# Optimization experiments

Hardware: AMD Instinct MI355X
Metric: run time of the kernel (lower is better)

The kernel has to match this reference:

```python
import jax, jax.numpy as jnp
import numpy as np

B, T, D = 32, 2048, 80
K1 = K2 = 3
S1 = S2 = 2
CB_DIM, CB_SIZE = 512, 1024
MASK_P = 0.1
NOISE_STD = 0.1
INPUT_DIM = D * K1 * K2  # 720


def _win_idx(T_in, k, s):
    Tp = (T_in - k) // s + 1
    return jnp.arange(Tp)[:, None] * s + jnp.arange(k)[None, :]  # (Tp, k)


def _unfold(x, k, s):
    # matches torch x.unfold(1, k, s).view(B, Tp, -1): out[b, t, f*k + j] = x[b, t*s + j, f]
    idx = _win_idx(x.shape[1], k, s)
    w = x[:, idx, :]                 # (B, Tp, k, F)
    w = jnp.swapaxes(w, 2, 3)        # (B, Tp, F, k)
    return w.reshape(w.shape[0], w.shape[1], -1)


def setup_inputs() -> dict:
    key = jax.random.key(0)
    k1, k2, k3, k4, k5 = jax.random.split(key, 5)
    raw_feats = jax.random.normal(k1, (B, T, D), jnp.float32)
    auged_feats = jax.random.normal(k2, (B, T, D), jnp.float32)
    length = jax.random.randint(k3, (B,), T // 2, T + 1)
    xav = (2.0 / (INPUT_DIM + CB_DIM)) ** 0.5  # xavier_normal std
    projector = jax.random.normal(k4, (INPUT_DIM, CB_DIM), jnp.float32) * xav
    codebook = jax.random.normal(k5, (CB_SIZE, CB_DIM), jnp.float32)
    return {"raw_feats": raw_feats, "auged_feats": auged_feats, "length": length,
            "projector": projector, "codebook": codebook}


def reference(raw_feats, auged_feats, length, projector, codebook):
    T1 = (T - K1) // S1 + 1
    T2 = (T1 - K2) // S2 + 1
    idx1 = _win_idx(T, K1, S1)                         # (T1, K1)
    idx2 = _win_idx(T1, K2, S2)                        # (T2, K2)
    frame_windows = idx1[idx2].reshape(T2, K1 * K2)    # (T2, 9) original frame idx per subsampled step
    label_lengths = ((length - K1) // S1 + 1 - K2) // S2 + 1  # (B,)

    # --- label path: two torch-style unfolds -> project -> nearest codebook entry ---
    stacked = _unfold(_unfold(raw_feats, K1, S1), K2, S2)     # (B, T2, 720)
    targets = jnp.matmul(stacked, projector)                  # (B, T2, 512)
    # squared-euclidean expansion; same argmin as ||t - c||
    dist = (jnp.sum(targets * targets, axis=-1, keepdims=True)
            - 2.0 * jnp.einsum('btd,cd->btc', targets, codebook)
            + jnp.sum(codebook * codebook, axis=-1))          # (B, T2, 1024)
    labels = jnp.argmin(dist, axis=-1) + 1                    # labels start from 1; 0 = ignore idx
    valid = jnp.arange(T2)[None, :] < label_lengths[:, None]  # (B, T2)
    labels = jnp.where(valid, labels, 0)[None]                # (num_codebooks=1, B, T2)

    # --- static (span length 1) random masking on valid subsampled steps ---
    mkey = jax.random.key(42)
    km, kn = jax.random.split(mkey)
    masked = (jax.random.uniform(km, (B, T2)) < MASK_P) & valid
    masked_dim = masked.astype(jnp.float32)                   # (B, T2)
    # scatter masked subsampled steps back onto original frame indices (union of windows)
    hits = jnp.zeros((B, T), jnp.float32).at[:, frame_windows].add(masked_dim[:, :, None])
    frame_mask = hits > 0                                     # (B, T)
    noise = NOISE_STD * jax.random.normal(kn, (B, T, D), auged_feats.dtype)
    masked_feats = jnp.where(frame_mask[:, :, None], noise, auged_feats)
    return masked_feats, labels, masked_dim
```

## Files before the change

### kernel.cpp

```cpp
#include <hip/hip_runtime.h>
#include <cstdint>

#define B_    32
#define T_    2048
#define D_    80
#define T2_   511
#define NROW  16352
#define GK    720
#define CBD   512
#define CBS   1024
#define HMASK 8176
#define HN    2621440
#define NP    16384
#define KB    23

using bfrag = __attribute__((ext_vector_type(8))) short;
using f32x4 = __attribute__((ext_vector_type(4))) float;
using s4    = __attribute__((ext_vector_type(4))) short;
using s8    = __attribute__((ext_vector_type(8))) short;

__device__ inline ushort f2bf(float f){
  uint32_t u = __float_as_uint(f);
  uint32_t r = (u + 0x7FFFu + ((u >> 16) & 1u)) >> 16;
  return (ushort)r;
}
__device__ inline float bf2f(ushort h){ return __uint_as_float(((uint32_t)h) << 16); }

#define GLL16(gsrc, ldst) __builtin_amdgcn_global_load_lds( \
    (__attribute__((address_space(1))) void*)(gsrc), \
    (__attribute__((address_space(3))) void*)(ldst), 16, 0, 0)

__host__ __device__ inline uint32_t rotl_(uint32_t v, int d){ return (v<<d)|(v>>(32-d)); }

__host__ __device__ inline void tf2x32(uint32_t k0, uint32_t k1, uint32_t& x0, uint32_t& x1){
  uint32_t ks2 = k0 ^ k1 ^ 0x1BD11BDAu;
  x0 += k0; x1 += k1;
  const int r0[4] = {13,15,26,6}, r1[4] = {17,29,16,24};
#pragma unroll
  for (int i=0;i<4;i++){ x0 += x1; x1 = rotl_(x1, r0[i]); x1 ^= x0; }
  x0 += k1; x1 += ks2 + 1u;
#pragma unroll
  for (int i=0;i<4;i++){ x0 += x1; x1 = rotl_(x1, r1[i]); x1 ^= x0; }
  x0 += ks2; x1 += k0 + 2u;
#pragma unroll
  for (int i=0;i<4;i++){ x0 += x1; x1 = rotl_(x1, r0[i]); x1 ^= x0; }
  x0 += k0; x1 += k1 + 3u;
#pragma unroll
  for (int i=0;i<4;i++){ x0 += x1; x1 = rotl_(x1, r1[i]); x1 ^= x0; }
  x0 += k1; x1 += ks2 + 4u;
#pragma unroll
  for (int i=0;i<4;i++){ x0 += x1; x1 = rotl_(x1, r0[i]); x1 ^= x0; }
  x0 += ks2; x1 += k0 + 5u;
}

__device__ inline float erfinv_f(float x){
  float w = -log1pf(-x*x);
  float p;
  if (w < 5.0f){
    w -= 2.5f;
    p = 2.81022636e-08f;
    p = fmaf(p, w, 3.43273939e-07f);
    p = fmaf(p, w, -3.5233877e-06f);
    p = fmaf(p, w, -4.39150654e-06f);
    p = fmaf(p, w, 0.00021858087f);
    p = fmaf(p, w, -0.00125372503f);
    p = fmaf(p, w, -0.00417768164f);
    p = fmaf(p, w, 0.246640727f);
    p = fmaf(p, w, 1.50140941f);
  } else {
    w = sqrtf(w) - 3.0f;
    p = -0.000200214257f;
    p = fmaf(p, w, 0.000100950558f);
    p = fmaf(p, w, 0.00134934322f);
    p = fmaf(p, w, -0.00367342844f);
    p = fmaf(p, w, 0.00573950773f);
    p = fmaf(p, w, -0.0076224613f);
    p = fmaf(p, w, 0.00943887047f);
    p = fmaf(p, w, 1.00167406f);
    p = fmaf(p, w, 2.83297682f);
  }
  return p * x;
}

__device__ inline int label_len(int L){ return (((L - 3) / 2) - 2) / 2 + 1; }

__global__ void cbnorm_k(const float* __restrict__ cb, ushort* __restrict__ W0, ushort* __restrict__ W1){
  int c = blockIdx.x, lane = threadIdx.x;
  double s = 0.0;
  for (int k = lane; k < CBD; k += 64){ float v = cb[c*CBD + k]; s += (double)v * (double)v; }
#pragma unroll
  for (int off = 32; off; off >>= 1) s += __shfl_down(s, off);
  float nf = (float)s;
  nf = __shfl(nf, 0);
  size_t base = ((size_t)(KB-1)*CBS + c)*32;
  int sw = ((c >> 1) & 3) << 3;
  if (lane == 16){
    float h = -0.5f * nf;
    ushort h0 = f2bf(h); ushort h1 = f2bf(h - bf2f(h0));
    W0[base + (16 ^ sw)] = h0; W1[base + (16 ^ sw)] = h1;
  } else if (lane > 16 && lane < 32){
    W0[base + (lane ^ sw)] = 0; W1[base + (lane ^ sw)] = 0;
  }
}

__global__ void gather_k(const float* __restrict__ raw, ushort* __restrict__ S0, ushort* __restrict__ S1){
  int idx = blockIdx.x * 256 + threadIdx.x;
  int g  = idx & 3;
  int n  = (idx >> 2) & (NP - 1);
  int kb = idx >> 16;
  int b = n / T2_, t2 = n - b * T2_;
  s8 o0, o1;
#pragma unroll
  for (int j = 0; j < 8; ++j){
    int k = kb*32 + g*8 + j;
    float v = 0.f;
    if (n < NROW){
      if (k < GK){
        int d = k / 9, rem = k - 9*d;
        int k1 = rem / 3, k2 = rem - 3*k1;
        int tm = 4*t2 + 2*k2 + k1;
        v = raw[(b * T_ + tm) * D_ + d];
      } else if (k == GK) v = 1.f;
    }
    ushort h0 = f2bf(v); ushort h1 = f2bf(v - bf2f(h0));
    o0[j] = (short)h0; o1[j] = (short)h1;
  }
  int gs = g ^ ((n >> 1) & 3);
  size_t off = ((size_t)kb*NP + n)*32 + gs*8;
  *(s8*)&S0[off] = o0;
  *(s8*)&S1[off] = o1;
}

__global__ __launch_bounds__(256) void wgemm_k(const float* __restrict__ P, const float* __restrict__ cb,
                                               float* __restrict__ Wp){
  __shared__ float sP[16][68];
  __shared__ float sC[16][68];
  int r0 = blockIdx.y * 64, c0 = blockIdx.x * 64;
  int kz = blockIdx.z;
  int tid = threadIdx.x, tx = tid & 15, ty = tid >> 4;
  float acc[4][4] = {};
  for (int k0 = kz * 128; k0 < kz * 128 + 128; k0 += 16){
    __syncthreads();
    {
      int r = tid >> 2, kq = tid & 3;
      int rr = r0 + r;
      float4 v = {0.f,0.f,0.f,0.f};
      if (rr < GK) v = *(const float4*)&P[rr * CBD + k0 + kq * 4];
      sP[kq*4+0][r] = v.x; sP[kq*4+1][r] = v.y; sP[kq*4+2][r] = v.z; sP[kq*4+3][r] = v.w;
      float4 w = *(const float4*)&cb[(c0 + r) * CBD + k0 + kq * 4];
      sC[kq*4+0][r] = w.x; sC[kq*4+1][r] = w.y; sC[kq*4+2][r] = w.z; sC[kq*4+3][r] = w.w;
    }
    __syncthreads();
#pragma unroll
    for (int kk = 0; kk < 16; ++kk){
      float4 a = *(const float4*)&sP[kk][ty * 4];
      float4 b = *(const float4*)&sC[kk][tx * 4];
      float av[4] = {a.x,a.y,a.z,a.w}, bv[4] = {b.x,b.y,b.z,b.w};
#pragma unroll
      for (int i = 0; i < 4; ++i)
#pragma unroll
        for (int j = 0; j < 4; ++j) acc[i][j] = fmaf(av[i], bv[j], acc[i][j]);
    }
  }
#pragma unroll
  for (int i = 0; i < 4; ++i){
    int r = r0 + ty * 4 + i;
    if (r < GK){
      float4 o; o.x = acc[i][0]; o.y = acc[i][1]; o.z = acc[i][2]; o.w = acc[i][3];
      *(float4*)&Wp[((size_t)kz * GK + r) * CBS + c0 + tx * 4] = o;
    }
  }
}

__global__ void wreduce_k(const float* __restrict__ Wp, ushort* __restrict__ W0, ushort* __restrict__ W1){
  int idx = blockIdx.x * 256 + threadIdx.x;
  int r = idx >> 10, c = idx & (CBS - 1);
  float v = Wp[(size_t)r * CBS + c]
          + Wp[((size_t)GK + r) * CBS + c]
          + Wp[((size_t)2*GK + r) * CBS + c]
          + Wp[((size_t)3*GK + r) * CBS + c];
  ushort h0 = f2bf(v); ushort h1 = f2bf(v - bf2f(h0));
  size_t o = ((size_t)(r >> 5) * CBS + c) * 32 + ((r & 31) ^ (((c >> 1) & 3) << 3));
  W0[o] = h0; W1[o] = h1;
}

__global__ __launch_bounds__(256, 1) void score_k(const ushort* __restrict__ S0, const ushort* __restrict__ S1,
                                                  const ushort* __restrict__ W0, const ushort* __restrict__ W1,
                                                  float* __restrict__ pval, int* __restrict__ pidx){
  extern __shared__ ushort lds[];
  int tid = threadIdx.x;
  int lane = tid & 63, wid = tid >> 6;
  int wm = wid >> 1, wn = wid & 1;
  int g = lane >> 4, lr = lane & 15;
  int gsw = g ^ ((lr >> 1) & 3);

  int id = blockIdx.x;
  int xcd = id & 7, slot = id >> 3;
  int cidx = slot & 3, ridx = (xcd << 3) | (slot >> 2);
  int n0 = ridx * 256, c0 = cidx * 256;

  const ushort* src0;
  size_t kstride;
  if      (wid == 0){ src0 = S0 + (size_t)n0*32; kstride = (size_t)NP*32; }
  else if (wid == 1){ src0 = S1 + (size_t)n0*32; kstride = (size_t)NP*32; }
  else if (wid == 2){ src0 = W0 + (size_t)c0*32; kstride = (size_t)CBS*32; }
  else              { src0 = W1 + (size_t)c0*32; kstride = (size_t)CBS*32; }

  f32x4 acc[8][8] = {};

  {
    ushort* dst = lds + (size_t)wid*8192;
#pragma unroll
    for (int q = 0; q < 16; ++q) GLL16(src0 + q*512 + lane*8, dst + q*512);
  }
  int buf = 0;
  for (int kb = 0; kb < KB; ++kb){
    if (kb + 1 < KB){
      const ushort* s = src0 + (size_t)(kb+1)*kstride;
      ushort* dst = lds + (size_t)((buf^1)*4 + wid)*8192;
#pragma unroll
      for (int q = 0; q < 16; ++q) GLL16(s + q*512 + lane*8, dst + q*512);
      asm volatile("s_waitcnt vmcnt(16)" ::: "memory");
    } else {
      asm volatile("s_waitcnt vmcnt(0)" ::: "memory");
    }
    __builtin_amdgcn_s_barrier();
    __builtin_amdgcn_sched_barrier(0);

    const ushort* A0 = lds + (size_t)(buf*4 + 0)*8192;
    const ushort* A1 = lds + (size_t)(buf*4 + 1)*8192;
    const ushort* B0 = lds + (size_t)(buf*4 + 2)*8192;
    const ushort* B1 = lds + (size_t)(buf*4 + 3)*8192;

    bfrag a0[8], a1[8], b0[8], b1[8];
#pragma unroll
    for (int mt = 0; mt < 8; ++mt){
      int off = (wm*128 + mt*16 + lr)*32 + gsw*8;
      a0[mt] = *(const bfrag*)&A0[off];
      a1[mt] = *(const bfrag*)&A1[off];
    }
#pragma unroll
    for (int nt = 0; nt < 8; ++nt){
      int off = (wn*128 + nt*16 + lr)*32 + gsw*8;
      b0[nt] = *(const bfrag*)&B0[off];
      b1[nt] = *(const bfrag*)&B1[off];
    }
#pragma unroll
    for (int mt = 0; mt < 8; ++mt)
#pragma unroll
      for (int nt = 0; nt < 8; ++nt){
        acc[mt][nt] = __builtin_amdgcn_mfma_f32_16x16x32_bf16(a0[mt], b0[nt], acc[mt][nt], 0,0,0);
        acc[mt][nt] = __builtin_amdgcn_mfma_f32_16x16x32_bf16(a0[mt], b1[nt], acc[mt][nt], 0,0,0);
        acc[mt][nt] = __builtin_amdgcn_mfma_f32_16x16x32_bf16(a1[mt], b0[nt], acc[mt][nt], 0,0,0);
      }
    __builtin_amdgcn_sched_barrier(0);
    __builtin_amdgcn_s_barrier();
    buf ^= 1;
  }

#pragma unroll
  for (int mt = 0; mt < 8; ++mt){
    float bv[4]; int bi[4];
#pragma unroll
    for (int r = 0; r < 4; ++r){
      float best = 3.4e38f; int besti = 0;
#pragma unroll
      for (int nt = 0; nt < 8; ++nt){
        float d = -2.f * acc[mt][nt][r];
        int c = c0 + wn*128 + nt*16 + lr;
        if (d < best){ best = d; besti = c; }
      }
      bv[r] = best; bi[r] = besti;
    }
#pragma unroll
    for (int off = 1; off < 16; off <<= 1){
#pragma unroll
      for (int r = 0; r < 4; ++r){
        float ov = __shfl_xor(bv[r], off);
        int   oi = __shfl_xor(bi[r], off);
        if (ov < bv[r] || (ov == bv[r] && oi < bi[r])){ bv[r] = ov; bi[r] = oi; }
      }
    }
    if (lr == 0){
      int p = cidx*2 + wn;
#pragma unroll
      for (int r = 0; r < 4; ++r){
        int n = n0 + wm*128 + mt*16 + g*4 + r;
        pval[(size_t)p*NP + n] = bv[r];
        pidx[(size_t)p*NP + n] = bi[r];
      }
    }
  }
}

__global__ void combine_k(const float* __restrict__ pval, const int* __restrict__ pidx,
                          const int* __restrict__ len, float* __restrict__ lb){
  int n = blockIdx.x * 256 + threadIdx.x;
  if (n >= NROW) return;
  float bv = pval[n]; int bi = pidx[n];
#pragma unroll
  for (int p = 1; p < 8; ++p){
    float v = pval[(size_t)p*NP + n]; int ii = pidx[(size_t)p*NP + n];
    if (v < bv || (v == bv && ii < bi)){ bv = v; bi = ii; }
  }
  int b = n / T2_, t2 = n - b * T2_;
  lb[n] = (t2 < label_len(len[b])) ? (float)(bi + 1) : 0.f;
}

__device__ inline void emit_mask(const int* len, float* md, int i, uint32_t bits){
  float u = __uint_as_float((bits >> 9) | 0x3F800000u) - 1.0f;
  int b = i / T2_, t2 = i - b * T2_;
  bool m = (u < 0.1f) && (t2 < label_len(len[b]));
  md[i] = m ? 1.0f : 0.0f;
}

__global__ void mask_k(const int* __restrict__ len, float* __restrict__ md, uint32_t km0, uint32_t km1){
  int j = blockIdx.x * 256 + threadIdx.x;
  if (j >= HMASK) return;
  uint32_t x0 = (uint32_t)j, x1 = (uint32_t)(j + HMASK);
  tf2x32(km0, km1, x0, x1);
  emit_mask(len, md, j, x0);
  emit_mask(len, md, j + HMASK, x1);
}

__device__ inline void emit_feat(const float* aug, const float* md, float* mf, int i, uint32_t bits){
  int tabs = i / D_;
  int t = tabs & (T_ - 1);
  int b = i / (D_ * T_);
  int lo = (t < 3) ? 0 : ((t - 3) >> 2);
  int hi = t >> 2; if (hi > T2_ - 1) hi = T2_ - 1;
  bool m = false;
  for (int t2 = lo; t2 <= hi; ++t2) m = m || (md[b * T2_ + t2] != 0.f);
  float v;
  if (m){
    float f = __uint_as_float((bits >> 9) | 0x3F800000u) - 1.0f;
    const float LOV = -0.99999994f;
    float u = fmaf(f, 2.0f, LOV);
    u = fmaxf(LOV, u);
    v = 0.1f * (1.41421356f * erfinv_f(u));
  } else {
    v = aug[i];
  }
  mf[i] = v;
}

__global__ void feats_k(const float* __restrict__ aug, const float* __restrict__ md,
                        float* __restrict__ mf, uint32_t kn0, uint32_t kn1){
  int j = blockIdx.x * 256 + threadIdx.x;
  uint32_t x0 = (uint32_t)j, x1 = (uint32_t)(j + HN);
  tf2x32(kn0, kn1, x0, x1);
  emit_feat(aug, md, mf, j, x0);
  emit_feat(aug, md, mf, j + HN, x1);
}

extern "C" void kernel_launch(void* const* d_in, const int* in_sizes, int n_in,
                              void* d_out, int out_size, void* d_ws, size_t ws_size,
                              hipStream_t stream){
  const float* raw  = (const float*)d_in[0];
  const float* aug  = (const float*)d_in[1];
  const int*   len  = (const int*)  d_in[2];
  const float* proj = (const float*)d_in[3];
  const float* cb   = (const float*)d_in[4];

  float* out = (float*)d_out;
  float* mf  = out;
  float* lb  = out + 5242880;
  float* md  = out + 5259232;

  ushort* w  = (ushort*)d_ws;
  ushort* W0 = w;
  ushort* W1 = W0 + (size_t)KB*CBS*32;
  ushort* S0 = W1 + (size_t)KB*CBS*32;
  ushort* S1 = S0 + (size_t)KB*NP*32;
  float* pval = (float*)(S1 + (size_t)KB*NP*32);
  int*   pidx = (int*)(pval + (size_t)16*NP);
  float* Wp   = (float*)(pidx + (size_t)16*NP);

  hipFuncSetAttribute((const void*)score_k, hipFuncAttributeMaxDynamicSharedMemorySize, 131072);

  uint32_t a0 = 0u, a1 = 2u, b0 = 1u, b1 = 3u;
  tf2x32(0u, 42u, a0, a1);
  tf2x32(0u, 42u, b0, b1);
  uint32_t km0 = a0, km1 = b0, kn0 = a1, kn1 = b1;

  cbnorm_k<<<CBS, 64, 0, stream>>>(cb, W0, W1);
  wgemm_k<<<dim3(CBS / 64, 12, 4), 256, 0, stream>>>(proj, cb, Wp);
  wreduce_k<<<(GK * CBS) / 256, 256, 0, stream>>>(Wp, W0, W1);
  gather_k<<<(KB * NP * 4) / 256, 256, 0, stream>>>(raw, S0, S1);
  score_k<<<256, 256, 131072, stream>>>(S0, S1, W0, W1, pval, pidx);
  combine_k<<<(NROW + 255) / 256, 256, 0, stream>>>(pval, pidx, len, lb);
  mask_k<<<(HMASK + 255) / 256, 256, 0, stream>>>(len, md, km0, km1);
  feats_k<<<HN / 256, 256, 0, stream>>>(aug, md, mf, kn0, kn1);
}
```

Baseline: 151.7 us.

## Split score kernel across 8 waves with halved per-wave N tile

Doubles the score kernel's block to 512 threads. Each wave now computes a 128x64 output sub-tile instead of 128x128, and two waves share each LDS staging load. Per-wave accumulator registers drop by half and more waves are available to hide latency. A-fragment loads move inside the mt loop. The extra column partition raises the partial-result count to 16, so combine_k reads twice as many candidates. The trade-off is more LDS reads of A, since each A fragment is reused over fewer columns.

```diff
diff --git a/kernel.cpp b/kernel.cpp
--- a/kernel.cpp
+++ b/kernel.cpp
@@ -184,13 +184,13 @@
   W0[o] = h0; W1[o] = h1;
 }
 
-__global__ __launch_bounds__(256, 1) void score_k(const ushort* __restrict__ S0, const ushort* __restrict__ S1,
+__global__ __launch_bounds__(512, 2) void score_k(const ushort* __restrict__ S0, const ushort* __restrict__ S1,
                                                   const ushort* __restrict__ W0, const ushort* __restrict__ W1,
                                                   float* __restrict__ pval, int* __restrict__ pidx){
   extern __shared__ ushort lds[];
   int tid = threadIdx.x;
   int lane = tid & 63, wid = tid >> 6;
-  int wm = wid >> 1, wn = wid & 1;
+  int wm = wid >> 2, wn = wid & 3;
   int g = lane >> 4, lr = lane & 15;
   int gsw = g ^ ((lr >> 1) & 3);
 
@@ -199,28 +199,30 @@
   int cidx = slot & 3, ridx = (xcd << 3) | (slot >> 2);
   int n0 = ridx * 256, c0 = cidx * 256;
 
+  int p = wid >> 1, h = wid & 1;
   const ushort* src0;
   size_t kstride;
-  if      (wid == 0){ src0 = S0 + (size_t)n0*32; kstride = (size_t)NP*32; }
-  else if (wid == 1){ src0 = S1 + (size_t)n0*32; kstride = (size_t)NP*32; }
-  else if (wid == 2){ src0 = W0 + (size_t)c0*32; kstride = (size_t)CBS*32; }
-  else              { src0 = W1 + (size_t)c0*32; kstride = (size_t)CBS*32; }
-
-  f32x4 acc[8][8] = {};
+  if      (p == 0){ src0 = S0 + (size_t)n0*32; kstride = (size_t)NP*32; }
+  else if (p == 1){ src0 = S1 + (size_t)n0*32; kstride = (size_t)NP*32; }
+  else if (p == 2){ src0 = W0 + (size_t)c0*32; kstride = (size_t)CBS*32; }
+  else            { src0 = W1 + (size_t)c0*32; kstride = (size_t)CBS*32; }
+  src0 += h * 4096;
+
+  f32x4 acc[8][4] = {};
 
   {
-    ushort* dst = lds + (size_t)wid*8192;
-#pragma unroll
-    for (int q = 0; q < 16; ++q) GLL16(src0 + q*512 + lane*8, dst + q*512);
+    ushort* dst = lds + (size_t)p*8192 + h*4096;
+#pragma unroll
+    for (int q = 0; q < 8; ++q) GLL16(src0 + q*512 + lane*8, dst + q*512);
   }
   int buf = 0;
   for (int kb = 0; kb < KB; ++kb){
     if (kb + 1 < KB){
       const ushort* s = src0 + (size_t)(kb+1)*kstride;
-      ushort* dst = lds + (size_t)((buf^1)*4 + wid)*8192;
-#pragma unroll
-      for (int q = 0; q < 16; ++q) GLL16(s + q*512 + lane*8, dst + q*512);
-      asm volatile("s_waitcnt vmcnt(16)" ::: "memory");
+      ushort* dst = lds + (size_t)((buf^1)*4 + p)*8192 + h*4096;
+#pragma unroll
+      for (int q = 0; q < 8; ++q) GLL16(s + q*512 + lane*8, dst + q*512);
+      asm volatile("s_waitcnt vmcnt(8)" ::: "memory");
     } else {
       asm volatile("s_waitcnt vmcnt(0)" ::: "memory");
     }
@@ -232,27 +234,25 @@
     const ushort* B0 = lds + (size_t)(buf*4 + 2)*8192;
     const ushort* B1 = lds + (size_t)(buf*4 + 3)*8192;
 
-    bfrag a0[8], a1[8], b0[8], b1[8];
+    bfrag b0[4], b1[4];
+#pragma unroll
+    for (int nt = 0; nt < 4; ++nt){
+      int off = (wn*64 + nt*16 + lr)*32 + gsw*8;
+      b0[nt] = *(const bfrag*)&B0[off];
+      b1[nt] = *(const bfrag*)&B1[off];
+    }
 #pragma unroll
     for (int mt = 0; mt < 8; ++mt){
       int off = (wm*128 + mt*16 + lr)*32 + gsw*8;
-      a0[mt] = *(const bfrag*)&A0[off];
-      a1[mt] = *(const bfrag*)&A1[off];
-    }
-#pragma unroll
-    for (int nt = 0; nt < 8; ++nt){
-      int off = (wn*128 + nt*16 + lr)*32 + gsw*8;
-      b0[nt] = *(const bfrag*)&B0[off];
-      b1[nt] = *(const bfrag*)&B1[off];
-    }
-#pragma unroll
-    for (int mt = 0; mt < 8; ++mt)
-#pragma unroll
-      for (int nt = 0; nt < 8; ++nt){
-        acc[mt][nt] = __builtin_amdgcn_mfma_f32_16x16x32_bf16(a0[mt], b0[nt], acc[mt][nt], 0,0,0);
-        acc[mt][nt] = __builtin_amdgcn_mfma_f32_16x16x32_bf16(a0[mt], b1[nt], acc[mt][nt], 0,0,0);
-        acc[mt][nt] = __builtin_amdgcn_mfma_f32_16x16x32_bf16(a1[mt], b0[nt], acc[mt][nt], 0,0,0);
+      bfrag a0 = *(const bfrag*)&A0[off];
+      bfrag a1 = *(const bfrag*)&A1[off];
+#pragma unroll
+      for (int nt = 0; nt < 4; ++nt){
+        acc[mt][nt] = __builtin_amdgcn_mfma_f32_16x16x32_bf16(a0, b0[nt], acc[mt][nt], 0,0,0);
+        acc[mt][nt] = __builtin_amdgcn_mfma_f32_16x16x32_bf16(a0, b1[nt], acc[mt][nt], 0,0,0);
+        acc[mt][nt] = __builtin_amdgcn_mfma_f32_16x16x32_bf16(a1, b0[nt], acc[mt][nt], 0,0,0);
       }
+    }
     __builtin_amdgcn_sched_barrier(0);
     __builtin_amdgcn_s_barrier();
     buf ^= 1;
@@ -265,9 +265,9 @@
     for (int r = 0; r < 4; ++r){
       float best = 3.4e38f; int besti = 0;
 #pragma unroll
-      for (int nt = 0; nt < 8; ++nt){
+      for (int nt = 0; nt < 4; ++nt){
         float d = -2.f * acc[mt][nt][r];
-        int c = c0 + wn*128 + nt*16 + lr;
+        int c = c0 + wn*64 + nt*16 + lr;
         if (d < best){ best = d; besti = c; }
       }
       bv[r] = best; bi[r] = besti;
@@ -282,12 +282,12 @@
       }
     }
     if (lr == 0){
-      int p = cidx*2 + wn;
+      int pp = cidx*4 + wn;
 #pragma unroll
       for (int r = 0; r < 4; ++r){
         int n = n0 + wm*128 + mt*16 + g*4 + r;
-        pval[(size_t)p*NP + n] = bv[r];
-        pidx[(size_t)p*NP + n] = bi[r];
+        pval[(size_t)pp*NP + n] = bv[r];
+        pidx[(size_t)pp*NP + n] = bi[r];
       }
     }
   }
@@ -299,7 +299,7 @@
   if (n >= NROW) return;
   float bv = pval[n]; int bi = pidx[n];
 #pragma unroll
-  for (int p = 1; p < 8; ++p){
+  for (int p = 1; p < 16; ++p){
     float v = pval[(size_t)p*NP + n]; int ii = pidx[(size_t)p*NP + n];
     if (v < bv || (v == bv && ii < bi)){ bv = v; bi = ii; }
   }
@@ -387,7 +387,7 @@
   wgemm_k<<<dim3(CBS / 64, 12, 4), 256, 0, stream>>>(proj, cb, Wp);
   wreduce_k<<<(GK * CBS) / 256, 256, 0, stream>>>(Wp, W0, W1);
   gather_k<<<(KB * NP * 4) / 256, 256, 0, stream>>>(raw, S0, S1);
-  score_k<<<256, 256, 131072, stream>>>(S0, S1, W0, W1, pval, pidx);
+  score_k<<<256, 512, 131072, stream>>>(S0, S1, W0, W1, pval, pidx);
   combine_k<<<(NROW + 255) / 256, 256, 0, stream>>>(pval, pidx, len, lb);
   mask_k<<<(HMASK + 255) / 256, 256, 0, stream>>>(len, md, km0, km1);
   feats_k<<<HN / 256, 256, 0, stream>>>(aug, md, mf, kn0, kn1);
```

Result: no change. 151.8 us (+0.1%).
